# Kernel optimization log

Hardware: AMD Instinct MI355X
Metric: run time of the kernel (lower is better)

The kernel has to match this reference:

```python
import jax, jax.numpy as jnp
import numpy as np

AGENT_RADIUS = 0.2
SAFETY_DIST = 0.1
_ang = np.linspace(0.0, 2.0 * np.pi, 8, endpoint=False)
OBSTACLES = np.stack([10.0 * np.cos(_ang), 10.0 * np.sin(_ang), 0.5 * np.ones(8)], axis=-1).astype(np.float32)  # (x, y, r)


def _qp_solve(p, G, h):
    """Exact solve of: min_z 0.5 z^T z + p^T z  s.t. G z <= h, z in R^2.
    Equivalent to QPFunction with Q=I. Enumerates KKT candidates over active
    sets of size 0, 1, 2 (closed form in 2D) and picks the feasible optimum.
    p: [2], G: [m,2], h: [m]."""
    m = G.shape[0]
    ii, jj = np.triu_indices(m, 1)
    # active set {} -> unconstrained minimizer
    z0 = -p[None, :]                                        # [1,2]
    # active set {i}: z = -p - lam*g_i, g_i.z = h_i
    gg = jnp.sum(G * G, axis=-1)                            # [m]
    lam1 = (-(G @ p) - h) / (gg + 1e-12)
    z1 = -p[None, :] - lam1[:, None] * G                    # [m,2]
    ok1 = lam1 >= -1e-8
    # active set {i,j}: z solves 2x2 system [g_i; g_j] z = [h_i; h_j]
    Gi, Gj = G[ii], G[jj]                                   # [P,2]
    hi, hj = h[ii], h[jj]
    det = Gi[:, 0] * Gj[:, 1] - Gi[:, 1] * Gj[:, 0]
    det_ok = jnp.abs(det) > 1e-9
    ds = jnp.where(det_ok, det, 1.0)
    zx = (hi * Gj[:, 1] - hj * Gi[:, 1]) / ds
    zy = (Gi[:, 0] * hj - Gj[:, 0] * hi) / ds
    z2 = jnp.stack([zx, zy], axis=-1)                       # [P,2]
    r = -(z2 + p[None, :])                                  # A^T lam = r
    lam_i = (Gj[:, 1] * r[:, 0] - Gj[:, 0] * r[:, 1]) / ds
    lam_j = (Gi[:, 0] * r[:, 1] - Gi[:, 1] * r[:, 0]) / ds
    ok2 = det_ok & (lam_i >= -1e-8) & (lam_j >= -1e-8)
    Z = jnp.concatenate([z0, z1, z2], axis=0)               # [K,2]
    ok = jnp.concatenate([jnp.ones((1,), bool), ok1, ok2], axis=0)
    tol = 1e-6 * (1.0 + jnp.abs(h))
    feas = jnp.all(Z @ G.T <= (h + tol)[None, :], axis=-1)  # [K]
    obj = 0.5 * jnp.sum(Z * Z, axis=-1) + Z @ p
    obj = jnp.where(ok & feas, obj, jnp.inf)
    return Z[jnp.argmin(obj)]


def _forward(x, mean, std, W1, b1, W21, b21, W31, b31, W22, b22, W32, b32):
    x0 = x * std + mean                                     # de-normalized state [B,8]
    hid = jax.nn.relu(x @ W1.T + b1)
    x31 = jax.nn.relu(hid @ W21.T + b21) @ W31.T + b31      # reference control p [B,2]
    x32 = 4.0 * jax.nn.sigmoid(jax.nn.relu(hid @ W22.T + b22) @ W32.T + b32)  # CBF penalties [B,2]
    px, py, theta, v = x0[:, 0], x0[:, 1], x0[:, 2], x0[:, 3]
    ox, oy, oth, ov = x0[:, 4], x0[:, 5], x0[:, 6], x0[:, 7]
    st, ct = jnp.sin(theta), jnp.cos(theta)
    vs, vc = v * st, v * ct
    obs = jnp.asarray(OBSTACLES, x.dtype)
    # static obstacle constraints, vectorized over the n_obs obstacles
    dx = px[:, None] - obs[None, :, 0]                      # [B,n_obs]
    dy = py[:, None] - obs[None, :, 1]
    R = AGENT_RADIUS + obs[:, 2] + SAFETY_DIST
    bar = dx * dx + dy * dy - (R * R)[None, :]
    bdot = 2.0 * dx * vc[:, None] + 2.0 * dy * vs[:, None]
    Lf2b = (2.0 * v * v)[:, None]
    u1 = -2.0 * dx * vs[:, None] + 2.0 * dy * vc[:, None]
    u2 = 2.0 * dx * ct[:, None] + 2.0 * dy * st[:, None]
    G_obs = -jnp.stack([u1, u2], axis=-1)                   # [B,n_obs,2]
    s0, s1 = x32[:, 0:1], x32[:, 1:2]
    h_obs = Lf2b + (s0 + s1) * bdot + (s0 * s1) * bar       # [B,n_obs]
    # opponent constraint
    Ro = 2.0 * AGENT_RADIUS + SAFETY_DIST
    dxo, dyo = px - ox, py - oy
    so, co = jnp.sin(oth), jnp.cos(oth)
    bar_o = dxo * dxo + dyo * dyo - Ro * Ro
    bdot_o = 2.0 * dxo * (vc - ov * co) + 2.0 * dyo * (vs - ov * so)
    Lf2b_o = 2.0 * (v * v + ov * ov + 2.0 * v * ov * jnp.cos(theta - oth))
    u1o = -2.0 * dxo * vs + 2.0 * dyo * vc
    u2o = 2.0 * dxo * ct + 2.0 * dyo * st
    G_opp = -jnp.stack([u1o, u2o], axis=-1)[:, None, :]     # [B,1,2]
    h_opp = (Lf2b_o + (x32[:, 0] + x32[:, 1]) * bdot_o + x32[:, 0] * x32[:, 1] * bar_o)[:, None]
    G = jnp.concatenate([G_obs, G_opp], axis=1)             # [B,m,2]
    h = jnp.concatenate([h_obs, h_opp], axis=1)             # [B,m]
    return jax.vmap(_qp_solve)(x31, G, h)                   # [B,2]


def setup_inputs() -> dict:
    key = jax.random.key(0)
    ks = jax.random.split(key, 6)
    B, nF, H1, H2 = 65536, 8, 256, 128

    def lin(k, o, i):
        k1, k2 = jax.random.split(k)
        W = jax.random.normal(k1, (o, i), jnp.float32) / np.float32(np.sqrt(i))
        b = jax.random.normal(k2, (o,), jnp.float32) * 0.01
        return W, b

    W1, b1 = lin(ks[0], H1, nF)
    W21, b21 = lin(ks[1], H2, H1)
    W31, b31 = lin(ks[2], 2, H2)
    W22, b22 = lin(ks[3], H2, H1)
    W32, b32 = lin(ks[4], 2, H2)
    x = jax.random.normal(ks[5], (B, nF), jnp.float32)
    return {"x": x, "mean": jnp.zeros((nF,), jnp.float32), "std": jnp.ones((nF,), jnp.float32),
            "W1": W1, "b1": b1, "W21": W21, "b21": b21, "W31": W31, "b31": b31,
            "W22": W22, "b22": b22, "W32": W32, "b32": b32, "sgn": 1}


def reference(x, mean, std, W1, b1, W21, b21, W31, b31, W22, b22, W32, b32, sgn):
    # sgn==1 / training path -> batched differentiable QP solve
    return _forward(x, mean, std, W1, b1, W21, b21, W31, b31, W22, b22, W32, b32)
```

## Files before the change

### kernel.cpp

```cpp
#include <hip/hip_runtime.h>
#include <hip/hip_bf16.h>
#include <math.h>


typedef unsigned int u32;
typedef unsigned long long u64;
typedef unsigned short u16;
typedef __attribute__((ext_vector_type(8))) short short8;
typedef __attribute__((ext_vector_type(4))) float f32x4;
typedef __attribute__((ext_vector_type(2))) float f32x2;
typedef __attribute__((ext_vector_type(4))) u32 u32x4;

union Frag { short8 v; u32 u[4]; u32x4 q; };

__device__ __forceinline__ u32 packbf(float a, float b) {
    float2 f2; f2.x = a; f2.y = b;
    __hip_bfloat162 h = __float22bfloat162_rn(f2);
    union { __hip_bfloat162 h2; u32 u; } cv; cv.h2 = h;
    return cv.u;
}

__device__ const float OBX[8] = { 10.f, 7.07106781186547524f, 6.123234e-16f, -7.07106781186547524f,
                                 -10.f, -7.07106781186547524f, -1.8369702e-15f, 7.07106781186547524f };
__device__ const float OBY[8] = { 0.f, 7.07106781186547524f, 10.f, 7.07106781186547524f,
                                  1.2246468e-15f, -7.07106781186547524f, -10.f, -7.07106781186547524f };

#define PI0_ 0x2111111100000000ULL
#define PI1_ 0x5544443333322222ULL
#define PI2_ 0x7665ULL
#define PJ0_ 0x3876543287654321ULL
#define PJ1_ 0x7687658765487654ULL
#define PJ2_ 0x8878ULL
__device__ __forceinline__ int unpack4(u64 w0, u64 w1, u64 w2, int t) {
    u64 w = (t < 16) ? w0 : (t < 32) ? w1 : w2;
    return (int)((w >> ((t & 15) * 4)) & 15);
}

__global__ __launch_bounds__(256)
void prep_kernel(const float* __restrict__ W21, const float* __restrict__ W22,
                 u32* __restrict__ ws)
{
    int idx  = blockIdx.x * 256 + threadIdx.x;
    int lane = idx & 63;
    int nt   = (idx >> 6) & 7;
    int ks   = (idx >> 9) & 7;
    int head = idx >> 12;
    const float* W = head ? W22 : W21;
    int n  = nt * 16 + (lane & 15);
    int k0 = ks * 32 + (lane >> 4) * 8;
    const float* s = W + n * 256 + k0;
    u32x4 o;
    o.x = packbf(s[0], s[1]);
    o.y = packbf(s[2], s[3]);
    o.z = packbf(s[4], s[5]);
    o.w = packbf(s[6], s[7]);
    __builtin_nontemporal_store(o, (u32x4*)ws + idx);
}

__global__ __launch_bounds__(256)
void barriernet_kernel(const float* __restrict__ x,
                       const float* __restrict__ meanp,
                       const float* __restrict__ stdp,
                       const float* __restrict__ W1,
                       const float* __restrict__ b1,
                       const float* __restrict__ b21,
                       const float* __restrict__ W31,
                       const float* __restrict__ b31,
                       const float* __restrict__ b22,
                       const float* __restrict__ W32,
                       const float* __restrict__ b32,
                       const u32* __restrict__ wsB,
                       float* __restrict__ out, int Btot)
{
    const int tid  = threadIdx.x;
    const int wave = tid >> 6;
    const int lane = tid & 63;
    const int q    = lane >> 4;
    const int m    = lane & 15;
    const int blockRow = blockIdx.x * 64;

    __shared__ u32x4 stage[2048];
    __shared__ float lds_p[64][4];

    f32x4 xa0, xb0;
    {
        int R0 = blockRow + wave * 16 + m;
        const f32x4* xv0 = (const f32x4*)(x + (R0 < Btot ? R0 : 0) * 8);
        xa0 = xv0[0]; xb0 = xv0[1];
    }

    const f32x4* W1v = (const f32x4*)W1;
    const f32x4* b1v = (const f32x4*)b1;

    Frag A[8];
    #pragma unroll
    for (int ks = 0; ks < 8; ++ks) {
        int kb = ks * 32 + q * 8;
        f32x4 bA = b1v[kb >> 2];
        f32x4 bB = b1v[(kb >> 2) + 1];
        float h0[8];
        #pragma unroll
        for (int j = 0; j < 8; ++j) {
            f32x4 wa = W1v[(kb + j) * 2];
            f32x4 wb = W1v[(kb + j) * 2 + 1];
            float a0 = (j < 4) ? bA[j] : bB[j - 4];
            a0 = fmaf(wa.x, xa0.x, a0);
            a0 = fmaf(wa.y, xa0.y, a0);
            a0 = fmaf(wa.z, xa0.z, a0);
            a0 = fmaf(wa.w, xa0.w, a0);
            a0 = fmaf(wb.x, xb0.x, a0);
            a0 = fmaf(wb.y, xb0.y, a0);
            a0 = fmaf(wb.z, xb0.z, a0);
            a0 = fmaf(wb.w, xb0.w, a0);
            h0[j] = fmaxf(a0, 0.f);
        }
        #pragma unroll
        for (int t = 0; t < 4; ++t)
            A[ks].u[t] = packbf(h0[2 * t], h0[2 * t + 1]);
    }

    const u32x4* wsB4 = (const u32x4*)wsB;

    #pragma unroll 1
    for (int head = 0; head < 2; ++head) {
        const float* b2 = head ? b22 : b21;
        const float* W3 = head ? W32 : W31;
        const float* b3 = head ? b32 : b31;

        f32x4 acc[8];
        #pragma unroll
        for (int nt = 0; nt < 8; ++nt) acc[nt] = (f32x4){0.f, 0.f, 0.f, 0.f};

        #pragma unroll
        for (int half = 0; half < 2; ++half) {
            const u32x4* src = wsB4 + head * 4096 + half * 2048;
            #pragma unroll
            for (int i = 0; i < 8; ++i) {
                int fi = (wave * 8 + i) * 64 + lane;
                stage[fi] = src[fi];
            }
            __syncthreads();
            #pragma unroll
            for (int ksl = 0; ksl < 4; ++ksl) {
                const int ks = half * 4 + ksl;
                Frag Bf[8];
                #pragma unroll
                for (int nt = 0; nt < 8; ++nt)
                    Bf[nt].q = stage[ksl * 512 + nt * 64 + lane];
                #pragma unroll
                for (int nt = 0; nt < 8; ++nt)
                    acc[nt] = __builtin_amdgcn_mfma_f32_16x16x32_bf16(A[ks].v, Bf[nt].v, acc[nt], 0, 0, 0);
            }
            __syncthreads();
        }

        float pr0[4], pr1[4];
        #pragma unroll
        for (int rg = 0; rg < 4; ++rg) { pr0[rg] = 0.f; pr1[rg] = 0.f; }
        #pragma unroll
        for (int nt = 0; nt < 8; ++nt) {
            int col = nt * 16 + m;
            float b2c = b2[col];
            float w0c = W3[col];
            float w1c = W3[128 + col];
            #pragma unroll
            for (int rg = 0; rg < 4; ++rg) {
                float rv = fmaxf(acc[nt][rg] + b2c, 0.f);
                pr0[rg] = fmaf(rv, w0c, pr0[rg]);
                pr1[rg] = fmaf(rv, w1c, pr1[rg]);
            }
        }
        #pragma unroll
        for (int rg = 0; rg < 4; ++rg) {
            float v0 = pr0[rg], v1 = pr1[rg];
            #pragma unroll
            for (int off = 1; off < 16; off <<= 1) {
                v0 += __shfl_xor(v0, off, 64);
                v1 += __shfl_xor(v1, off, 64);
            }
            pr0[rg] = v0; pr1[rg] = v1;
        }
        if (m == 0) {
            #pragma unroll
            for (int rg = 0; rg < 4; ++rg) {
                int row = wave * 16 + q * 4 + rg;
                float a0 = pr0[rg] + b3[0];
                float a1 = pr1[rg] + b3[1];
                if (head == 0) {
                    lds_p[row][0] = a0;
                    lds_p[row][1] = a1;
                } else {
                    lds_p[row][2] = 4.f / (1.f + __expf(-a0));
                    lds_p[row][3] = 4.f / (1.f + __expf(-a1));
                }
            }
        }
    }
    __syncthreads();

    f32x4 (*qC)[64]  = (f32x4(*)[64])stage;
    f32x4 (*res)[64] = (f32x4(*)[64])(stage + 576);

    const int rq   = tid & 63;
    const int part = tid >> 6;
    const int R    = blockRow + rq;
    float p0 = lds_p[rq][0];
    float p1 = lds_p[rq][1];

    if (part == 0) {
        float s0 = lds_p[rq][2];
        float s1 = lds_p[rq][3];
        float xr[8];
        const float* xp = x + (R < Btot ? R : 0) * 8;
        #pragma unroll
        for (int c = 0; c < 8; ++c) xr[c] = fmaf(xp[c], stdp[c], meanp[c]);
        float px = xr[0], py = xr[1], th = xr[2], v = xr[3];
        float ox = xr[4], oy = xr[5], oth = xr[6], ov = xr[7];
        float st = __sinf(th),  ct = __cosf(th);
        float so = __sinf(oth), co = __cosf(oth);
        float vs = v * st, vc = v * ct;
        float sps = s0 + s1, ss = s0 * s1;
        float Lf2b = 2.f * v * v;
        #pragma unroll 1
        for (int k = 0; k < 8; ++k) {
            float dx = px - OBX[k], dy = py - OBY[k];
            float bar  = dx * dx + dy * dy - 0.64f;
            float bdot = 2.f * dx * vc + 2.f * dy * vs;
            float gx = 2.f * dx * vs - 2.f * dy * vc;
            float gy = -(2.f * dx * ct + 2.f * dy * st);
            float hk = Lf2b + sps * bdot + ss * bar;
            float ht = hk + 1e-6f * (1.f + fabsf(hk));
            qC[k][rq] = (f32x4){gx, gy, hk, ht};
        }
        {
            float dxo = px - ox, dyo = py - oy;
            float bar_o  = dxo * dxo + dyo * dyo - 0.25f;
            float bdot_o = 2.f * dxo * (vc - ov * co) + 2.f * dyo * (vs - ov * so);
            float Lf2b_o = 2.f * (v * v + ov * ov + 2.f * v * ov * __cosf(th - oth));
            float gx = 2.f * dxo * vs - 2.f * dyo * vc;
            float gy = -(2.f * dxo * ct + 2.f * dyo * st);
            float hk = Lf2b_o + sps * bdot_o + ss * bar_o;
            float ht = hk + 1e-6f * (1.f + fabsf(hk));
            qC[8][rq] = (f32x4){gx, gy, hk, ht};
        }
    }
    __syncthreads();

    const f32x4 C0 = qC[0][rq], C1 = qC[1][rq], C2 = qC[2][rq];
    const f32x4 C3 = qC[3][rq], C4 = qC[4][rq], C5 = qC[5][rq];
    const f32x4 C6 = qC[6][rq], C7 = qC[7][rq], C8 = qC[8][rq];

    const int c0i = (part == 0) ? 0  : (part == 1) ? 12 : (part == 2) ? 24 : 35;
    const int c1i = (part == 0) ? 12 : (part == 1) ? 24 : (part == 2) ? 35 : 46;
    float bobj = INFINITY;
    float bzx = -p0, bzy = -p1;
    #pragma unroll 2
    for (int c = c0i; c < c1i; ++c) {
        float zx, zy;
        bool pre;
        if (c == 0) {
            zx = -p0; zy = -p1; pre = true;
        } else if (c <= 9) {
            f32x4 g = qC[c - 1][rq];
            float gg  = g.x * g.x + g.y * g.y;
            float lam = (-(g.x * p0 + g.y * p1) - g.z) / (gg + 1e-12f);
            zx = -p0 - lam * g.x;
            zy = -p1 - lam * g.y;
            pre = (lam >= -1e-8f);
        } else {
            int t = c - 10;
            int pi = unpack4(PI0_, PI1_, PI2_, t);
            int pj = unpack4(PJ0_, PJ1_, PJ2_, t);
            f32x4 gi = qC[pi][rq];
            f32x4 gj = qC[pj][rq];
            float det = gi.x * gj.y - gi.y * gj.x;
            bool dok = fabsf(det) > 1e-9f;
            float ds = dok ? det : 1.0f;
            float inv = 1.0f / ds;
            zx = (gi.z * gj.y - gj.z * gi.y) * inv;
            zy = (gi.x * gj.z - gj.x * gi.z) * inv;
            float rx = -(zx + p0), ry = -(zy + p1);
            float li = (gj.y * rx - gj.x * ry) * inv;
            float lj = (gi.x * ry - gi.y * rx) * inv;
            pre = dok && (li >= -1e-8f) && (lj >= -1e-8f);
        }
        bool ok = pre;
        ok = ok && (zx * C0.x + zy * C0.y <= C0.w);
        ok = ok && (zx * C1.x + zy * C1.y <= C1.w);
        ok = ok && (zx * C2.x + zy * C2.y <= C2.w);
        ok = ok && (zx * C3.x + zy * C3.y <= C3.w);
        ok = ok && (zx * C4.x + zy * C4.y <= C4.w);
        ok = ok && (zx * C5.x + zy * C5.y <= C5.w);
        ok = ok && (zx * C6.x + zy * C6.y <= C6.w);
        ok = ok && (zx * C7.x + zy * C7.y <= C7.w);
        ok = ok && (zx * C8.x + zy * C8.y <= C8.w);
        float obj = 0.5f * (zx * zx + zy * zy) + zx * p0 + zy * p1;
        if (ok && obj < bobj) { bobj = obj; bzx = zx; bzy = zy; }
    }

    if (part) {
        res[part - 1][rq] = (f32x4){bobj, bzx, bzy, 0.f};
    }
    __syncthreads();
    if (part == 0) {
        #pragma unroll
        for (int pp = 0; pp < 3; ++pp) {
            f32x4 r = res[pp][rq];
            if (r.x < bobj) { bobj = r.x; bzx = r.y; bzy = r.z; }
        }
        if (R < Btot) {
            f32x2 o2; o2.x = bzx; o2.y = bzy;
            ((f32x2*)out)[R] = o2;
        }
    }
}

extern "C" void kernel_launch(void* const* d_in, const int* in_sizes, int n_in,
                              void* d_out, int out_size, void* d_ws, size_t ws_size,
                              hipStream_t stream) {
    const float* x    = (const float*)d_in[0];
    const float* mean = (const float*)d_in[1];
    const float* stdv = (const float*)d_in[2];
    const float* W1   = (const float*)d_in[3];
    const float* b1   = (const float*)d_in[4];
    const float* W21  = (const float*)d_in[5];
    const float* b21  = (const float*)d_in[6];
    const float* W31  = (const float*)d_in[7];
    const float* b31  = (const float*)d_in[8];
    const float* W22  = (const float*)d_in[9];
    const float* b22  = (const float*)d_in[10];
    const float* W32  = (const float*)d_in[11];
    const float* b32  = (const float*)d_in[12];
    int B = in_sizes[0] / 8;
    float* out = (float*)d_out;
    u32* ws = (u32*)d_ws;

    hipLaunchKernelGGL(prep_kernel, dim3(32), dim3(256), 0, stream, W21, W22, ws);

    hipLaunchKernelGGL(barriernet_kernel, dim3((B + 63) / 64), dim3(256), 0, stream,
                       x, mean, stdv, W1, b1, b21, W31, b31, b22, W32, b32,
                       ws, out, B);
}
```

Measured before the change: 119.7 us.

## Process 256 rows per block with 4 M-tiles per wave and per-thread QP

Each block now handles 256 rows instead of 64. Each wave computes four 16-row M-tiles, so every staged W2 B-fragment in LDS is reused across four MFMAs, and the LDS staging cost per row drops. The QP enumeration is no longer split across four threads per row. Each thread now runs all 46 candidates for its own row, which removes the extra barrier and the cross-part min reduction. In exchange, register pressure is much higher (the launch bounds are raised to min 1 block) and there are four times fewer blocks, so occupancy and latency hiding may suffer.

```diff
diff --git a/kernel.cpp b/kernel.cpp
--- a/kernel.cpp
+++ b/kernel.cpp
@@ -57,7 +57,7 @@
     __builtin_nontemporal_store(o, (u32x4*)ws + idx);
 }
 
-__global__ __launch_bounds__(256)
+__global__ __launch_bounds__(256, 1)
 void barriernet_kernel(const float* __restrict__ x,
                        const float* __restrict__ meanp,
                        const float* __restrict__ stdp,
@@ -77,46 +77,53 @@
     const int lane = tid & 63;
     const int q    = lane >> 4;
     const int m    = lane & 15;
-    const int blockRow = blockIdx.x * 64;
-
-    __shared__ u32x4 stage[2048];
-    __shared__ float lds_p[64][4];
-
-    f32x4 xa0, xb0;
-    {
-        int R0 = blockRow + wave * 16 + m;
-        const f32x4* xv0 = (const f32x4*)(x + (R0 < Btot ? R0 : 0) * 8);
-        xa0 = xv0[0]; xb0 = xv0[1];
+    const int blockRow = blockIdx.x * 256;
+
+    __shared__ u32x4 smem[2304];
+    __shared__ float lds_p[256][4];
+
+    f32x4 xa[4], xb[4];
+    #pragma unroll
+    for (int mt = 0; mt < 4; ++mt) {
+        int R0 = blockRow + wave * 64 + mt * 16 + m;
+        const f32x4* xv = (const f32x4*)(x + (R0 < Btot ? R0 : 0) * 8);
+        xa[mt] = xv[0]; xb[mt] = xv[1];
     }
 
     const f32x4* W1v = (const f32x4*)W1;
     const f32x4* b1v = (const f32x4*)b1;
 
-    Frag A[8];
+    Frag A[4][8];
     #pragma unroll
     for (int ks = 0; ks < 8; ++ks) {
         int kb = ks * 32 + q * 8;
         f32x4 bA = b1v[kb >> 2];
         f32x4 bB = b1v[(kb >> 2) + 1];
-        float h0[8];
+        float h[4][8];
         #pragma unroll
         for (int j = 0; j < 8; ++j) {
             f32x4 wa = W1v[(kb + j) * 2];
             f32x4 wb = W1v[(kb + j) * 2 + 1];
-            float a0 = (j < 4) ? bA[j] : bB[j - 4];
-            a0 = fmaf(wa.x, xa0.x, a0);
-            a0 = fmaf(wa.y, xa0.y, a0);
-            a0 = fmaf(wa.z, xa0.z, a0);
-            a0 = fmaf(wa.w, xa0.w, a0);
-            a0 = fmaf(wb.x, xb0.x, a0);
-            a0 = fmaf(wb.y, xb0.y, a0);
-            a0 = fmaf(wb.z, xb0.z, a0);
-            a0 = fmaf(wb.w, xb0.w, a0);
-            h0[j] = fmaxf(a0, 0.f);
-        }
-        #pragma unroll
-        for (int t = 0; t < 4; ++t)
-            A[ks].u[t] = packbf(h0[2 * t], h0[2 * t + 1]);
+            float bj = (j < 4) ? bA[j] : bB[j - 4];
+            #pragma unroll
+            for (int mt = 0; mt < 4; ++mt) {
+                float a0 = bj;
+                a0 = fmaf(wa.x, xa[mt].x, a0);
+                a0 = fmaf(wa.y, xa[mt].y, a0);
+                a0 = fmaf(wa.z, xa[mt].z, a0);
+                a0 = fmaf(wa.w, xa[mt].w, a0);
+                a0 = fmaf(wb.x, xb[mt].x, a0);
+                a0 = fmaf(wb.y, xb[mt].y, a0);
+                a0 = fmaf(wb.z, xb[mt].z, a0);
+                a0 = fmaf(wb.w, xb[mt].w, a0);
+                h[mt][j] = fmaxf(a0, 0.f);
+            }
+        }
+        #pragma unroll
+        for (int mt = 0; mt < 4; ++mt)
+            #pragma unroll
+            for (int t = 0; t < 4; ++t)
+                A[mt][ks].u[t] = packbf(h[mt][2 * t], h[mt][2 * t + 1]);
     }
 
     const u32x4* wsB4 = (const u32x4*)wsB;
@@ -127,17 +134,19 @@
         const float* W3 = head ? W32 : W31;
         const float* b3 = head ? b32 : b31;
 
-        f32x4 acc[8];
-        #pragma unroll
-        for (int nt = 0; nt < 8; ++nt) acc[nt] = (f32x4){0.f, 0.f, 0.f, 0.f};
+        f32x4 acc[4][8];
+        #pragma unroll
+        for (int mt = 0; mt < 4; ++mt)
+            #pragma unroll
+            for (int nt = 0; nt < 8; ++nt) acc[mt][nt] = (f32x4){0.f, 0.f, 0.f, 0.f};
 
         #pragma unroll
         for (int half = 0; half < 2; ++half) {
             const u32x4* src = wsB4 + head * 4096 + half * 2048;
             #pragma unroll
             for (int i = 0; i < 8; ++i) {
-                int fi = (wave * 8 + i) * 64 + lane;
-                stage[fi] = src[fi];
+                int fi = i * 256 + tid;
+                smem[fi] = src[fi];
             }
             __syncthreads();
             #pragma unroll
@@ -146,17 +155,23 @@
                 Frag Bf[8];
                 #pragma unroll
                 for (int nt = 0; nt < 8; ++nt)
-                    Bf[nt].q = stage[ksl * 512 + nt * 64 + lane];
-                #pragma unroll
-                for (int nt = 0; nt < 8; ++nt)
-                    acc[nt] = __builtin_amdgcn_mfma_f32_16x16x32_bf16(A[ks].v, Bf[nt].v, acc[nt], 0, 0, 0);
+                    Bf[nt].q = smem[ksl * 512 + nt * 64 + lane];
+                #pragma unroll
+                for (int nt = 0; nt < 8; ++nt) {
+                    #pragma unroll
+                    for (int mt = 0; mt < 4; ++mt)
+                        acc[mt][nt] = __builtin_amdgcn_mfma_f32_16x16x32_bf16(
+                            A[mt][ks].v, Bf[nt].v, acc[mt][nt], 0, 0, 0);
+                }
             }
             __syncthreads();
         }
 
-        float pr0[4], pr1[4];
-        #pragma unroll
-        for (int rg = 0; rg < 4; ++rg) { pr0[rg] = 0.f; pr1[rg] = 0.f; }
+        float pr0[4][4], pr1[4][4];
+        #pragma unroll
+        for (int mt = 0; mt < 4; ++mt)
+            #pragma unroll
+            for (int rg = 0; rg < 4; ++rg) { pr0[mt][rg] = 0.f; pr1[mt][rg] = 0.f; }
         #pragma unroll
         for (int nt = 0; nt < 8; ++nt) {
             int col = nt * 16 + m;
@@ -164,52 +179,57 @@
             float w0c = W3[col];
             float w1c = W3[128 + col];
             #pragma unroll
+            for (int mt = 0; mt < 4; ++mt) {
+                #pragma unroll
+                for (int rg = 0; rg < 4; ++rg) {
+                    float rv = fmaxf(acc[mt][nt][rg] + b2c, 0.f);
+                    pr0[mt][rg] = fmaf(rv, w0c, pr0[mt][rg]);
+                    pr1[mt][rg] = fmaf(rv, w1c, pr1[mt][rg]);
+                }
+            }
+        }
+        #pragma unroll
+        for (int mt = 0; mt < 4; ++mt) {
+            #pragma unroll
             for (int rg = 0; rg < 4; ++rg) {
-                float rv = fmaxf(acc[nt][rg] + b2c, 0.f);
-                pr0[rg] = fmaf(rv, w0c, pr0[rg]);
-                pr1[rg] = fmaf(rv, w1c, pr1[rg]);
-            }
-        }
-        #pragma unroll
-        for (int rg = 0; rg < 4; ++rg) {
-            float v0 = pr0[rg], v1 = pr1[rg];
-            #pragma unroll
-            for (int off = 1; off < 16; off <<= 1) {
-                v0 += __shfl_xor(v0, off, 64);
-                v1 += __shfl_xor(v1, off, 64);
-            }
-            pr0[rg] = v0; pr1[rg] = v1;
+                float v0 = pr0[mt][rg], v1 = pr1[mt][rg];
+                #pragma unroll
+                for (int off = 1; off < 16; off <<= 1) {
+                    v0 += __shfl_xor(v0, off, 64);
+                    v1 += __shfl_xor(v1, off, 64);
+                }
+                pr0[mt][rg] = v0; pr1[mt][rg] = v1;
+            }
         }
         if (m == 0) {
             #pragma unroll
-            for (int rg = 0; rg < 4; ++rg) {
-                int row = wave * 16 + q * 4 + rg;
-                float a0 = pr0[rg] + b3[0];
-                float a1 = pr1[rg] + b3[1];
-                if (head == 0) {
-                    lds_p[row][0] = a0;
-                    lds_p[row][1] = a1;
-                } else {
-                    lds_p[row][2] = 4.f / (1.f + __expf(-a0));
-                    lds_p[row][3] = 4.f / (1.f + __expf(-a1));
+            for (int mt = 0; mt < 4; ++mt) {
+                #pragma unroll
+                for (int rg = 0; rg < 4; ++rg) {
+                    int row = wave * 64 + mt * 16 + q * 4 + rg;
+                    float a0 = pr0[mt][rg] + b3[0];
+                    float a1 = pr1[mt][rg] + b3[1];
+                    if (head == 0) {
+                        lds_p[row][0] = a0;
+                        lds_p[row][1] = a1;
+                    } else {
+                        lds_p[row][2] = 4.f / (1.f + __expf(-a0));
+                        lds_p[row][3] = 4.f / (1.f + __expf(-a1));
+                    }
                 }
             }
         }
     }
     __syncthreads();
 
-    f32x4 (*qC)[64]  = (f32x4(*)[64])stage;
-    f32x4 (*res)[64] = (f32x4(*)[64])(stage + 576);
-
-    const int rq   = tid & 63;
-    const int part = tid >> 6;
-    const int R    = blockRow + rq;
-    float p0 = lds_p[rq][0];
-    float p1 = lds_p[rq][1];
-
-    if (part == 0) {
-        float s0 = lds_p[rq][2];
-        float s1 = lds_p[rq][3];
+    f32x4 (*qC)[256] = (f32x4(*)[256])smem;
+
+    const int R = blockRow + tid;
+    float p0 = lds_p[tid][0];
+    float p1 = lds_p[tid][1];
+    {
+        float s0 = lds_p[tid][2];
+        float s1 = lds_p[tid][3];
         float xr[8];
         const float* xp = x + (R < Btot ? R : 0) * 8;
         #pragma unroll
@@ -230,7 +250,7 @@
             float gy = -(2.f * dx * ct + 2.f * dy * st);
             float hk = Lf2b + sps * bdot + ss * bar;
             float ht = hk + 1e-6f * (1.f + fabsf(hk));
-            qC[k][rq] = (f32x4){gx, gy, hk, ht};
+            qC[k][tid] = (f32x4){gx, gy, hk, ht};
         }
         {
             float dxo = px - ox, dyo = py - oy;
@@ -241,27 +261,23 @@
             float gy = -(2.f * dxo * ct + 2.f * dyo * st);
             float hk = Lf2b_o + sps * bdot_o + ss * bar_o;
             float ht = hk + 1e-6f * (1.f + fabsf(hk));
-            qC[8][rq] = (f32x4){gx, gy, hk, ht};
-        }
-    }
-    __syncthreads();
-
-    const f32x4 C0 = qC[0][rq], C1 = qC[1][rq], C2 = qC[2][rq];
-    const f32x4 C3 = qC[3][rq], C4 = qC[4][rq], C5 = qC[5][rq];
-    const f32x4 C6 = qC[6][rq], C7 = qC[7][rq], C8 = qC[8][rq];
-
-    const int c0i = (part == 0) ? 0  : (part == 1) ? 12 : (part == 2) ? 24 : 35;
-    const int c1i = (part == 0) ? 12 : (part == 1) ? 24 : (part == 2) ? 35 : 46;
+            qC[8][tid] = (f32x4){gx, gy, hk, ht};
+        }
+    }
+    const f32x4 C0 = qC[0][tid], C1 = qC[1][tid], C2 = qC[2][tid];
+    const f32x4 C3 = qC[3][tid], C4 = qC[4][tid], C5 = qC[5][tid];
+    const f32x4 C6 = qC[6][tid], C7 = qC[7][tid], C8 = qC[8][tid];
+
     float bobj = INFINITY;
     float bzx = -p0, bzy = -p1;
     #pragma unroll 2
-    for (int c = c0i; c < c1i; ++c) {
+    for (int c = 0; c < 46; ++c) {
         float zx, zy;
         bool pre;
         if (c == 0) {
             zx = -p0; zy = -p1; pre = true;
         } else if (c <= 9) {
-            f32x4 g = qC[c - 1][rq];
+            f32x4 g = qC[c - 1][tid];
             float gg  = g.x * g.x + g.y * g.y;
             float lam = (-(g.x * p0 + g.y * p1) - g.z) / (gg + 1e-12f);
             zx = -p0 - lam * g.x;
@@ -271,8 +287,8 @@
             int t = c - 10;
             int pi = unpack4(PI0_, PI1_, PI2_, t);
             int pj = unpack4(PJ0_, PJ1_, PJ2_, t);
-            f32x4 gi = qC[pi][rq];
-            f32x4 gj = qC[pj][rq];
+            f32x4 gi = qC[pi][tid];
+            f32x4 gj = qC[pj][tid];
             float det = gi.x * gj.y - gi.y * gj.x;
             bool dok = fabsf(det) > 1e-9f;
             float ds = dok ? det : 1.0f;
@@ -298,20 +314,9 @@
         if (ok && obj < bobj) { bobj = obj; bzx = zx; bzy = zy; }
     }
 
-    if (part) {
-        res[part - 1][rq] = (f32x4){bobj, bzx, bzy, 0.f};
-    }
-    __syncthreads();
-    if (part == 0) {
-        #pragma unroll
-        for (int pp = 0; pp < 3; ++pp) {
-            f32x4 r = res[pp][rq];
-            if (r.x < bobj) { bobj = r.x; bzx = r.y; bzy = r.z; }
-        }
-        if (R < Btot) {
-            f32x2 o2; o2.x = bzx; o2.y = bzy;
-            ((f32x2*)out)[R] = o2;
-        }
+    if (R < Btot) {
+        f32x2 o2; o2.x = bzx; o2.y = bzy;
+        ((f32x2*)out)[R] = o2;
     }
 }
 
@@ -337,7 +342,7 @@
 
     hipLaunchKernelGGL(prep_kernel, dim3(32), dim3(256), 0, stream, W21, W22, ws);
 
-    hipLaunchKernelGGL(barriernet_kernel, dim3((B + 63) / 64), dim3(256), 0, stream,
+    hipLaunchKernelGGL(barriernet_kernel, dim3((B + 255) / 256), dim3(256), 0, stream,
                        x, mean, stdv, W1, b1, b21, W31, b31, b22, W32, b32,
                        ws, out, B);
 }
```

After: 121.3 us. No clear change (+1.4%).
